# Kernel optimization log

Hardware: AMD Instinct MI355X
Metric: run time of the kernel (lower is better)

## Reference

```python
import jax, jax.numpy as jnp
import numpy as np

B, S, N, IN_DIM = 64, 12, 170, 1
E, L, C, H, OUT = 128, 4, 2, 8, 1
OFFSET, PAD = 0, 1          # seq_offset=0 -> Conv2d padding (0,1)
LOOKUP, MAXLEN = 0, 100
EPS = 1e-5


def _shift(x, s):
    """y[:, i] = x[:, i+s] along axis 1, zero padded."""
    if s == 0:
        return x
    z = jnp.zeros_like(x[:, :abs(s)])
    if s > 0:
        return jnp.concatenate([x[:, s:], z], axis=1)
    return jnp.concatenate([z, x[:, :s]], axis=1)


def _masked_conv_diag(x, w):
    """Diagonal of Conv2d(kernel=(1,3), pad=(0,PAD)) applied to the causally
    masked repeated tensor, computed directly without the O(B*S*S*E) blowup:
      out[b,i] = sum_k W[:,:,k] @ (mask(i, i+k-PAD) * x[b, i+k-PAD])
    where mask(i,j) = (j <= i) or (j < OFFSET)."""
    i = jnp.arange(x.shape[1])
    out = None
    for k in range(3):
        s = k - PAD
        term = jnp.einsum('bse,oe->bso', _shift(x, s), w[:, :, k])
        if s > 0:  # only future taps can be masked out
            term = term * (i + s < OFFSET).astype(x.dtype)[None, :, None]
        out = term if out is None else out + term
    return out


def _conv1d_k3(x, w, b):
    """Conv1d over the seq dim, kernel 3, padding 1, with bias. x:[b,s,e]."""
    out = b
    for k in range(3):
        out = out + jnp.einsum('bse,oe->bso', _shift(x, k - 1), w[:, :, k])
    return out


def _layer_norm(x, g, b):
    m = jnp.mean(x, -1, keepdims=True)
    v = jnp.mean((x - m) ** 2, -1, keepdims=True)
    return (x - m) * jax.lax.rsqrt(v + EPS) * g + b


def _mha(q_in, kv_in, w, b, mask=None):
    dh = E // H
    q = (q_in @ w[0] + b[0]).reshape(q_in.shape[0], q_in.shape[1], H, dh)
    k = (kv_in @ w[1] + b[1]).reshape(kv_in.shape[0], kv_in.shape[1], H, dh)
    v = (kv_in @ w[2] + b[2]).reshape(kv_in.shape[0], kv_in.shape[1], H, dh)
    s = jnp.einsum('bqhd,bkhd->bhqk', q, k) * np.float32(1.0 / np.sqrt(dh))
    if mask is not None:
        s = jnp.where(mask[None, None], s, jnp.float32(-1e9))
    a = jax.nn.softmax(s, axis=-1)
    o = jnp.einsum('bhqk,bkhd->bqhd', a, v).reshape(q_in.shape[0], q_in.shape[1], E)
    return o @ w[3] + b[3]


def setup_inputs() -> dict:
    key = jax.random.key(0)
    ks = jax.random.split(key, 16)

    def nrm(k, shape, scale=0.05):
        return scale * jax.random.normal(k, shape, dtype=jnp.float32)

    # sinusoidal positional table, length MAXLEN
    pos = np.arange(MAXLEN)[:, None].astype(np.float32)
    div = np.exp(-np.log(10000.0) * np.arange(0, E, 2) / E).astype(np.float32)
    pe = np.zeros((MAXLEN, E), np.float32)
    pe[:, 0::2] = np.sin(pos * div)
    pe[:, 1::2] = np.cos(pos * div)

    return {
        'x': jax.random.normal(ks[0], (B, S, N, IN_DIM), jnp.float32),
        'enc_x': jax.random.normal(ks[1], (C, B * N, S, E), jnp.float32),
        'tgt_mask': jnp.tril(jnp.ones((S, S), bool)),
        'emb_w': nrm(ks[2], (IN_DIM, E), 1.0),
        'emb_b': jnp.zeros((E,), jnp.float32),
        'pe': jnp.asarray(pe),
        'conv_q_w': nrm(ks[3], (L, E, E, 3)),
        'conv_k_w': nrm(ks[4], (L, C, E, E, 3)),
        'conv_k_b': jnp.zeros((L, C, E), jnp.float32),
        'sa_w': nrm(ks[5], (L, 4, E, E)),
        'sa_b': jnp.zeros((L, 4, E), jnp.float32),
        'ca_w': nrm(ks[6], (L, C, 4, E, E)),
        'ca_b': jnp.zeros((L, C, 4, E), jnp.float32),
        'ff_w1': nrm(ks[7], (L, E, 4 * E)),
        'ff_b1': jnp.zeros((L, 4 * E), jnp.float32),
        'ff_w2': nrm(ks[8], (L, 4 * E, E)),
        'ff_b2': jnp.zeros((L, E), jnp.float32),
        'ln_g': jnp.ones((L, 3, E), jnp.float32),
        'ln_b': jnp.zeros((L, 3, E), jnp.float32),
        'fc_w': nrm(ks[9], (E, OUT)),
        'fc_b': jnp.zeros((OUT,), jnp.float32),
    }


def reference(x, enc_x, tgt_mask, emb_w, emb_b, pe, conv_q_w, conv_k_w, conv_k_b,
              sa_w, sa_b, ca_w, ca_b, ff_w1, ff_b1, ff_w2, ff_b2, ln_g, ln_b,
              fc_w, fc_b):
    h = x @ emb_w + emb_b                                    # [B,S,N,E]
    h = jnp.transpose(h, (1, 0, 2, 3)).reshape(S, B * N, E)  # [S,B*N,E]
    h = jnp.transpose(h, (1, 0, 2))                          # [B*N,S,E]
    h = h + pe[LOOKUP:LOOKUP + S]
    for l in range(L):
        # local trends: causal masked-conv query (the fused diagonal)
        h = _masked_conv_diag(h, conv_q_w[l])
        enc_list = [_conv1d_k3(enc_x[i], conv_k_w[l, i], conv_k_b[l, i])
                    for i in range(C)]
        # decoder block: self-attn -> cross-attn (avg over features) -> FFN
        h = _layer_norm(h + _mha(h, h, sa_w[l], sa_b[l], tgt_mask),
                        ln_g[l, 0], ln_b[l, 0])
        cross = sum(_mha(h, enc_list[i], ca_w[l, i], ca_b[l, i])
                    for i in range(C)) / C
        h = _layer_norm(h + cross, ln_g[l, 1], ln_b[l, 1])
        f = jax.nn.relu(h @ ff_w1[l] + ff_b1[l]) @ ff_w2[l] + ff_b2[l]
        h = _layer_norm(h + f, ln_g[l, 2], ln_b[l, 2])
    out = h @ fc_w + fc_b                                    # [B*N,S,OUT]
    out = jnp.transpose(out, (1, 0, 2)).reshape(S, B, N, OUT)
    return jnp.transpose(out, (1, 0, 2, 3))                  # [B,S,N,OUT]
```

## Files before the change

### kernel.cpp

```cpp
#include <hip/hip_runtime.h>


#define B_   64
#define S_   12
#define N_   170
#define BN_  (B_*N_)
#define E_   128
#define L_   4
#define C_   2
#define H_   8
#define DH_  16
#define FF_  512
#define EPS_ 1e-5f
#define THREADS 256

typedef unsigned short u16;
typedef __attribute__((ext_vector_type(4))) float f32x4;
typedef __attribute__((ext_vector_type(8))) u16   us8;
typedef __attribute__((ext_vector_type(4))) u16   us4;
typedef __attribute__((ext_vector_type(8))) __bf16 bf16x8;
union FragU { us8 u; bf16x8 b; };

__device__ __forceinline__ u16 f2bf(float f) {
    __bf16 h = (__bf16)f;
    return __builtin_bit_cast(u16, h);
}
__device__ __forceinline__ float bf2f(u16 s) {
    return __builtin_bit_cast(float, (unsigned)s << 16);
}

__global__ void k_encbf(const float* __restrict__ src, u16* __restrict__ dst, int n8) {
    int i = blockIdx.x * 256 + threadIdx.x;
    if (i < n8) {
        const f32x4 v0 = ((const f32x4*)src)[i*2];
        const f32x4 v1 = ((const f32x4*)src)[i*2 + 1];
        us8 w;
        w[0]=f2bf(v0[0]); w[1]=f2bf(v0[1]); w[2]=f2bf(v0[2]); w[3]=f2bf(v0[3]);
        w[4]=f2bf(v1[0]); w[5]=f2bf(v1[1]); w[6]=f2bf(v1[2]); w[7]=f2bf(v1[3]);
        ((us8*)dst)[i] = w;
    }
}

__global__ void k_wpack(const float* __restrict__ cq, const float* __restrict__ sa,
                        const float* __restrict__ ck, const float* __restrict__ ca,
                        const float* __restrict__ f1, const float* __restrict__ f2,
                        u16* __restrict__ wp) {
    int f  = blockIdx.x * 256 + threadIdx.x;
    int l  = f / 57344, fl = f % 57344;
    const float* src; int sk, so, KS, q;
    if (fl < 4096)        { int tap = fl >> 11; q = fl & 2047; KS = 4;
                            src = cq + (size_t)l*49152 + tap;            sk = 3;   so = 384; }
    else if (fl < 12288)  { int j = (fl - 4096) >> 11; q = fl & 2047; KS = 4;
                            src = sa + (size_t)(l*4 + j)*16384;          sk = 128; so = 1;   }
    else if (fl < 24576)  { int ct = (fl - 12288) >> 11; q = fl & 2047; KS = 4;
                            int ci = ct / 3, tap = ct % 3;
                            src = ck + (size_t)(l*2 + ci)*49152 + tap;   sk = 3;   so = 384; }
    else if (fl < 40960)  { int cj = (fl - 24576) >> 11; q = fl & 2047; KS = 4;
                            src = ca + (size_t)(l*8 + cj)*16384;         sk = 128; so = 1;   }
    else if (fl < 49152)  { q = fl - 40960; KS = 4;
                            src = f1 + (size_t)l*65536;                  sk = 512; so = 1;   }
    else                  { q = fl - 49152; KS = 16;
                            src = f2 + (size_t)l*65536;                  sk = 128; so = 1;   }
    int lane = q & 63, tt = q >> 6;
    int ks = tt % KS, ntile = tt / KS;
    int k0 = ks*32 + ((lane >> 4) << 3);
    int o  = ntile*16 + (lane & 15);
    us8 w;
    #pragma unroll
    for (int i = 0; i < 8; i++) w[i] = f2bf(src[(size_t)(k0 + i)*sk + (size_t)o*so]);
    *(us8*)(wp + (size_t)f*8) = w;
}

__device__ __forceinline__ void zero_pad_rows(u16* dst, int t) {
    if (t < 128) {
        int chunk = t & 15, ridx = t >> 4;
        int row = 12 + (ridx & 3) + ((ridx >> 2) << 4);
        us8 z = {0,0,0,0,0,0,0,0};
        *(us8*)((char*)dst + (((row << 8) + (chunk << 4)) ^ ((row & 7) << 4))) = z;
    }
}

__device__ __forceinline__ void stage24_bf(const u16* __restrict__ src, u16* dst, int t) {
    for (int i = t; i < 384; i += THREADS) {
        us8 v = ((const us8*)src)[i];
        int row = i >> 4;
        int g = row / 12, s = row - g*12;
        int rowT = g*16 + s;
        int colb = (i & 15) << 4;
        *(us8*)((char*)dst + (((rowT << 8) + colb) ^ ((rowT & 7) << 4))) = v;
    }
    zero_pad_rows(dst, t);
}

__device__ __forceinline__ void stage24_embed(const float* __restrict__ x,
    const float* __restrict__ ew, const float* __restrict__ eb,
    const float* __restrict__ pe, int bn0, u16* dst, int t) {
    #pragma unroll
    for (int it = 0; it < 3; it++) {
        int i = t + it*THREADS;
        int elem = i << 2;
        int srow = elem >> 7;
        int g = srow / 12, s = srow - g*12;
        int row = g*16 + s;
        int col = elem & 127;
        int bn = bn0 + g, b = bn / N_, n = bn - b*N_;
        float xv = x[(b*S_ + s)*N_ + n];
        const f32x4 w  = *(const f32x4*)(ew + col);
        const f32x4 bb = *(const f32x4*)(eb + col);
        const f32x4 p  = *(const f32x4*)(pe + s*E_ + col);
        us4 o; o[0] = f2bf(xv*w[0] + bb[0] + p[0]); o[1] = f2bf(xv*w[1] + bb[1] + p[1]);
               o[2] = f2bf(xv*w[2] + bb[2] + p[2]); o[3] = f2bf(xv*w[3] + bb[3] + p[3]);
        *(us4*)((char*)dst + (((row << 8) + (col << 1)) ^ ((row & 7) << 4))) = o;
    }
    zero_pad_rows(dst, t);
}

__device__ __forceinline__ void acc_init(f32x4 (&acc)[2][2], const float* bias, int wave, int lane) {
    #pragma unroll
    for (int nt = 0; nt < 2; nt++) {
        float bv = bias ? bias[(wave*2 + nt)*16 + (lane & 15)] : 0.f;
        #pragma unroll
        for (int mt = 0; mt < 2; mt++) {
            acc[mt][nt][0] = bv; acc[mt][nt][1] = bv; acc[mt][nt][2] = bv; acc[mt][nt][3] = bv;
        }
    }
}

__device__ __forceinline__ bf16x8 ldA(const u16* A, int row, int colb) {
    FragU fu; fu.u = *(const us8*)((const char*)A + (((row << 8) + colb) ^ ((row & 7) << 4)));
    return fu.b;
}

template<int KSTOT>
__device__ __forceinline__ void gemm24(const u16* A, const us8* __restrict__ WP, int ksOff,
                                       f32x4 (&acc)[2][2], int wave, int lane) {
    #pragma unroll
    for (int ks = 0; ks < 4; ks++) {
        int colb = (ks*32 + ((lane >> 4) << 3)) << 1;
        bf16x8 a[2];
        #pragma unroll
        for (int mt = 0; mt < 2; mt++) a[mt] = ldA(A, mt*16 + (lane & 15), colb);
        #pragma unroll
        for (int nt = 0; nt < 2; nt++) {
            FragU fb; fb.u = WP[((wave*2 + nt)*KSTOT + ksOff + ks)*64 + lane];
            #pragma unroll
            for (int mt = 0; mt < 2; mt++)
                acc[mt][nt] = __builtin_amdgcn_mfma_f32_16x16x32_bf16(a[mt], fb.b, acc[mt][nt], 0, 0, 0);
        }
    }
}

__device__ __forceinline__ void gemm24_rows(const u16* A, const int (&sr)[2],
                                            const us8* __restrict__ WP,
                                            f32x4 (&acc)[2][2], int wave, int lane) {
    #pragma unroll
    for (int ks = 0; ks < 4; ks++) {
        int colb = (ks*32 + ((lane >> 4) << 3)) << 1;
        bf16x8 a[2];
        #pragma unroll
        for (int mt = 0; mt < 2; mt++) a[mt] = ldA(A, sr[mt], colb);
        #pragma unroll
        for (int nt = 0; nt < 2; nt++) {
            FragU fb; fb.u = WP[((wave*2 + nt)*4 + ks)*64 + lane];
            #pragma unroll
            for (int mt = 0; mt < 2; mt++)
                acc[mt][nt] = __builtin_amdgcn_mfma_f32_16x16x32_bf16(a[mt], fb.b, acc[mt][nt], 0, 0, 0);
        }
    }
}

__device__ __forceinline__ void gemm24_x3(const u16* A,
        const us8* __restrict__ B0, const us8* __restrict__ B1, const us8* __restrict__ B2,
        f32x4 (&c0)[2][2], f32x4 (&c1)[2][2], f32x4 (&c2)[2][2], int wave, int lane) {
    #pragma unroll
    for (int ks = 0; ks < 4; ks++) {
        int colb = (ks*32 + ((lane >> 4) << 3)) << 1;
        bf16x8 a[2];
        #pragma unroll
        for (int mt = 0; mt < 2; mt++) a[mt] = ldA(A, mt*16 + (lane & 15), colb);
        #pragma unroll
        for (int nt = 0; nt < 2; nt++) {
            int bi = ((wave*2 + nt)*4 + ks)*64 + lane;
            FragU f0, f1, f2; f0.u = B0[bi]; f1.u = B1[bi]; f2.u = B2[bi];
            #pragma unroll
            for (int mt = 0; mt < 2; mt++) {
                c0[mt][nt] = __builtin_amdgcn_mfma_f32_16x16x32_bf16(a[mt], f0.b, c0[mt][nt], 0, 0, 0);
                c1[mt][nt] = __builtin_amdgcn_mfma_f32_16x16x32_bf16(a[mt], f1.b, c1[mt][nt], 0, 0, 0);
                c2[mt][nt] = __builtin_amdgcn_mfma_f32_16x16x32_bf16(a[mt], f2.b, c2[mt][nt], 0, 0, 0);
            }
        }
    }
}

__device__ __forceinline__ void gemm24_x2(const u16* A,
        const us8* __restrict__ B0, const us8* __restrict__ B1,
        f32x4 (&c0)[2][2], f32x4 (&c1)[2][2], int wave, int lane) {
    #pragma unroll
    for (int ks = 0; ks < 4; ks++) {
        int colb = (ks*32 + ((lane >> 4) << 3)) << 1;
        bf16x8 a[2];
        #pragma unroll
        for (int mt = 0; mt < 2; mt++) a[mt] = ldA(A, mt*16 + (lane & 15), colb);
        #pragma unroll
        for (int nt = 0; nt < 2; nt++) {
            int bi = ((wave*2 + nt)*4 + ks)*64 + lane;
            FragU f0, f1; f0.u = B0[bi]; f1.u = B1[bi];
            #pragma unroll
            for (int mt = 0; mt < 2; mt++) {
                c0[mt][nt] = __builtin_amdgcn_mfma_f32_16x16x32_bf16(a[mt], f0.b, c0[mt][nt], 0, 0, 0);
                c1[mt][nt] = __builtin_amdgcn_mfma_f32_16x16x32_bf16(a[mt], f1.b, c1[mt][nt], 0, 0, 0);
            }
        }
    }
}

template<bool RELU>
__device__ __forceinline__ void acc_store_bf(const f32x4 (&acc)[2][2], u16* Bp, int wave, int lane) {
    #pragma unroll
    for (int mt = 0; mt < 2; mt++)
    #pragma unroll
    for (int nt = 0; nt < 2; nt++)
    #pragma unroll
    for (int r = 0; r < 4; r++) {
        int row = mt*16 + ((lane >> 4) << 2) + r;
        int col = (wave*2 + nt)*16 + (lane & 15);
        float v = acc[mt][nt][r];
        if (RELU) v = fmaxf(v, 0.f);
        *(u16*)((char*)Bp + (((row << 8) + (col << 1)) ^ ((row & 7) << 4))) = f2bf(v);
    }
}

__device__ __forceinline__ void ld16(const u16* Bf, int row, int colb, float* o16) {
    int x = (row & 7) << 4;
    int base = (row << 8) + colb;
    us8 u0 = *(const us8*)((const char*)Bf + (base ^ x));
    us8 u1 = *(const us8*)((const char*)Bf + ((base + 16) ^ x));
    #pragma unroll
    for (int d = 0; d < 8; d++) { o16[d] = bf2f(u0[d]); o16[8+d] = bf2f(u1[d]); }
}

template<bool MASK>
__device__ __forceinline__ void attn24(u16* QA, const u16* KB, const u16* VB, int t) {
    if (t < 192) {
        int g = t / 96, rem = t % 96;
        int hh = rem / 12, qi = rem % 12;
        int hb2 = hh << 5;
        int rq = g*16 + qi;
        float qv[16]; ld16(QA, rq, hb2, qv);
        float sc[12]; float mx = -1e30f;
        #pragma unroll
        for (int j = 0; j < 12; j++) {
            float kv[16]; ld16(KB, g*16 + j, hb2, kv);
            float s = 0.f;
            #pragma unroll
            for (int d = 0; d < 16; d++) s += qv[d]*kv[d];
            s *= 0.25f;
            if (MASK && j > qi) s = -1e30f;
            sc[j] = s; mx = fmaxf(mx, s);
        }
        float sum = 0.f;
        #pragma unroll
        for (int j = 0; j < 12; j++) { sc[j] = __expf(sc[j] - mx); sum += sc[j]; }
        float inv = 1.f/sum;
        float ov[16];
        #pragma unroll
        for (int d = 0; d < 16; d++) ov[d] = 0.f;
        #pragma unroll
        for (int j = 0; j < 12; j++) {
            float vv[16]; ld16(VB, g*16 + j, hb2, vv);
            #pragma unroll
            for (int d = 0; d < 16; d++) ov[d] += sc[j]*vv[d];
        }
        int x = (rq & 7) << 4;
        us8 w0, w1;
        #pragma unroll
        for (int d = 0; d < 8; d++) { w0[d] = f2bf(ov[d]*inv); w1[d] = f2bf(ov[8+d]*inv); }
        *(us8*)((char*)QA + (((rq << 8) + hb2) ^ x))      = w0;
        *(us8*)((char*)QA + (((rq << 8) + hb2 + 16) ^ x)) = w1;
    }
}

__device__ __forceinline__ void ln_inreg(f32x4 (&v)[2][2], float* lnbuf,
                                         const float* __restrict__ g, const float* __restrict__ bb,
                                         int wave, int lane) {
    float gc[2], bc[2];
    #pragma unroll
    for (int nt = 0; nt < 2; nt++) {
        int col = (wave*2 + nt)*16 + (lane & 15);
        gc[nt] = g[col]; bc[nt] = bb[col];
    }
    #pragma unroll
    for (int mt = 0; mt < 2; mt++)
    #pragma unroll
    for (int r = 0; r < 4; r++) {
        float a = v[mt][0][r], c = v[mt][1][r];
        float p = a + c, q = a*a + c*c;
        #pragma unroll
        for (int off = 1; off < 16; off <<= 1) { p += __shfl_xor(p, off); q += __shfl_xor(q, off); }
        if ((lane & 15) == 0) {
            int row = mt*16 + ((lane >> 4) << 2) + r;
            lnbuf[(row*4 + wave)*2]     = p;
            lnbuf[(row*4 + wave)*2 + 1] = q;
        }
    }
    __syncthreads();
    #pragma unroll
    for (int mt = 0; mt < 2; mt++)
    #pragma unroll
    for (int r = 0; r < 4; r++) {
        int row = mt*16 + ((lane >> 4) << 2) + r;
        float sum = 0.f, ss = 0.f;
        #pragma unroll
        for (int w2 = 0; w2 < 4; w2++) { sum += lnbuf[(row*4 + w2)*2]; ss += lnbuf[(row*4 + w2)*2 + 1]; }
        float m   = sum * (1.f/128.f);
        float var = ss * (1.f/128.f) - m*m;
        float inv = rsqrtf(var + EPS_);
        #pragma unroll
        for (int nt = 0; nt < 2; nt++)
            v[mt][nt][r] = (v[mt][nt][r] - m)*inv*gc[nt] + bc[nt];
    }
}

template<bool EMB, bool FIN>
__global__ void __launch_bounds__(THREADS, 2)
k_layer(u16* __restrict__ hb, const float* __restrict__ x,
        const float* __restrict__ ew, const float* __restrict__ ebp, const float* __restrict__ pe,
        const u16* __restrict__ encb, const u16* __restrict__ lw,
        const float* __restrict__ sab, const float* __restrict__ ckb, const float* __restrict__ cab,
        const float* __restrict__ fb1, const float* __restrict__ fb2,
        const float* __restrict__ lg, const float* __restrict__ lb,
        const float* __restrict__ fcw, const float* __restrict__ fcb,
        float* __restrict__ outp) {
    __shared__ __align__(16) u16 P0[4096], P1[4096], P2[4096], P3[4096], P4[4096];
    float* lnbuf = (float*)P2;

    int t = threadIdx.x, wave = t >> 6, lane = t & 63;
    int bid = blockIdx.x;
    u16* hp = hb + (size_t)(bid*2) * (S_*E_);

    if (EMB) stage24_embed(x, ew, ebp, pe, bid*2, P0, t);
    else     stage24_bf(hp, P0, t);
    stage24_bf(encb + (size_t)(bid*2) * (S_*E_), P4, t);
    __syncthreads();

    int rr = lane & 15;
    int srp[2], srf[2], srn[2];
    #pragma unroll
    for (int mt = 0; mt < 2; mt++) {
        srp[mt] = (rr >= 1)     ? mt*16 + rr - 1 : mt*16 + 12;
        srf[mt] = mt*16 + rr;
        srn[mt] = (rr + 1 < 12) ? mt*16 + rr + 1 : mt*16 + 12;
    }

    f32x4 cacc[2][2];
    acc_init(cacc, nullptr, wave, lane);
    gemm24_rows(P0, srp, (const us8*)lw,           cacc, wave, lane);
    gemm24_rows(P0, srf, (const us8*)(lw + 16384), cacc, wave, lane);
    acc_store_bf<false>(cacc, P1, wave, lane);
    __syncthreads();

    {
        const us8* sap = (const us8*)(lw + 32768);
        f32x4 aq[2][2], ak[2][2], av[2][2];
        acc_init(aq, sab,       wave, lane);
        acc_init(ak, sab + 128, wave, lane);
        acc_init(av, sab + 256, wave, lane);
        gemm24_x3(P1, sap, sap + 2048, sap + 4096, aq, ak, av, wave, lane);
        acc_store_bf<false>(aq, P0, wave, lane);
        acc_store_bf<false>(ak, P2, wave, lane);
        acc_store_bf<false>(av, P3, wave, lane);
    }
    __syncthreads();
    attn24<true>(P0, P2, P3, t);
    __syncthreads();

    f32x4 hres[2][2];
    {
        f32x4 a[2][2];
        acc_init(a, sab + 384, wave, lane);
        gemm24<4>(P0, (const us8*)(lw + 81920), 0, a, wave, lane);
        #pragma unroll
        for (int mt = 0; mt < 2; mt++)
        #pragma unroll
        for (int nt = 0; nt < 2; nt++) hres[mt][nt] = a[mt][nt] + cacc[mt][nt];
    }
    ln_inreg(hres, lnbuf, lg, lb, wave, lane);
    acc_store_bf<false>(hres, P1, wave, lane);
    {
        const us8* ckp = (const us8*)(lw + 98304);
        f32x4 a[2][2];
        acc_init(a, ckb, wave, lane);
        gemm24_rows(P4, srp, ckp,        a, wave, lane);
        gemm24_rows(P4, srf, ckp + 2048, a, wave, lane);
        gemm24_rows(P4, srn, ckp + 4096, a, wave, lane);
        acc_store_bf<false>(a, P3, wave, lane);
    }
    __syncthreads();

    f32x4 creg[2][2];
    #pragma unroll
    for (int nt = 0; nt < 2; nt++) {
        int col = (wave*2 + nt)*16 + (lane & 15);
        float bv = cab[3*128 + col] + cab[7*128 + col];
        #pragma unroll
        for (int mt = 0; mt < 2; mt++) { creg[mt][nt][0]=bv; creg[mt][nt][1]=bv; creg[mt][nt][2]=bv; creg[mt][nt][3]=bv; }
    }

    const us8* cap0 = (const us8*)(lw + 196608);
    {
        f32x4 aq[2][2], ak[2][2], av[2][2];
        acc_init(aq, cab, wave, lane);
        gemm24<4>(P1, cap0, 0, aq, wave, lane);
        acc_store_bf<false>(aq, P0, wave, lane);
        acc_init(ak, cab + 128, wave, lane);
        acc_init(av, cab + 256, wave, lane);
        gemm24_x2(P3, cap0 + 2048, cap0 + 4096, ak, av, wave, lane);
        acc_store_bf<false>(ak, P2, wave, lane);
        acc_store_bf<false>(av, P4, wave, lane);
    }
    __syncthreads();
    stage24_bf(encb + ((size_t)BN_ + bid*2) * (S_*E_), P3, t);
    attn24<false>(P0, P2, P4, t);
    __syncthreads();

    gemm24<4>(P0, cap0 + 6144, 0, creg, wave, lane);
    {
        const us8* ckp = (const us8*)(lw + 98304 + 3*16384);
        f32x4 a[2][2];
        acc_init(a, ckb + 128, wave, lane);
        gemm24_rows(P3, srp, ckp,        a, wave, lane);
        gemm24_rows(P3, srf, ckp + 2048, a, wave, lane);
        gemm24_rows(P3, srn, ckp + 4096, a, wave, lane);
        acc_store_bf<false>(a, P4, wave, lane);
    }
    __syncthreads();

    const us8* cap1 = (const us8*)(lw + 196608 + 4*16384);
    {
        f32x4 aq[2][2], ak[2][2], av[2][2];
        acc_init(aq, cab + 4*128, wave, lane);
        gemm24<4>(P1, cap1, 0, aq, wave, lane);
        acc_store_bf<false>(aq, P0, wave, lane);
        acc_init(ak, cab + 5*128, wave, lane);
        acc_init(av, cab + 6*128, wave, lane);
        gemm24_x2(P4, cap1 + 2048, cap1 + 4096, ak, av, wave, lane);
        acc_store_bf<false>(ak, P2, wave, lane);
        acc_store_bf<false>(av, P3, wave, lane);
    }
    __syncthreads();
    attn24<false>(P0, P2, P3, t);
    __syncthreads();

    gemm24<4>(P0, cap1 + 6144, 0, creg, wave, lane);
    #pragma unroll
    for (int mt = 0; mt < 2; mt++)
    #pragma unroll
    for (int nt = 0; nt < 2; nt++) hres[mt][nt] = hres[mt][nt] + 0.5f*creg[mt][nt];
    ln_inreg(hres, lnbuf, lg + 128, lb + 128, wave, lane);
    acc_store_bf<false>(hres, P1, wave, lane);
    __syncthreads();

    f32x4 ffacc[2][2];
    acc_init(ffacc, fb2, wave, lane);
    #pragma unroll
    for (int half = 0; half < 2; half++) {
        {
            f32x4 a[2][2];
            acc_init(a, fb1 + (half*2)*128, wave, lane);
            gemm24<4>(P1, (const us8*)(lw + 327680) + (half*2)*2048, 0, a, wave, lane);
            acc_store_bf<true>(a, P2, wave, lane);
        }
        {
            f32x4 a[2][2];
            acc_init(a, fb1 + (half*2 + 1)*128, wave, lane);
            gemm24<4>(P1, (const us8*)(lw + 327680) + (half*2 + 1)*2048, 0, a, wave, lane);
            acc_store_bf<true>(a, P3, wave, lane);
        }
        __syncthreads();
        gemm24<16>(P2, (const us8*)(lw + 393216), (half*2)*4,     ffacc, wave, lane);
        gemm24<16>(P3, (const us8*)(lw + 393216), (half*2 + 1)*4, ffacc, wave, lane);
        __syncthreads();
    }
    #pragma unroll
    for (int mt = 0; mt < 2; mt++)
    #pragma unroll
    for (int nt = 0; nt < 2; nt++) hres[mt][nt] = hres[mt][nt] + ffacc[mt][nt];
    ln_inreg(hres, lnbuf, lg + 256, lb + 256, wave, lane);

    if (FIN) {
        float fw[2];
        #pragma unroll
        for (int nt = 0; nt < 2; nt++) fw[nt] = fcw[(wave*2 + nt)*16 + (lane & 15)];
        float pr[2][4];
        #pragma unroll
        for (int mt = 0; mt < 2; mt++)
        #pragma unroll
        for (int r = 0; r < 4; r++) {
            float p = hres[mt][0][r]*fw[0] + hres[mt][1][r]*fw[1];
            #pragma unroll
            for (int off = 1; off < 16; off <<= 1) p += __shfl_xor(p, off);
            pr[mt][r] = p;
        }
        __syncthreads();
        if ((lane & 15) == 0) {
            #pragma unroll
            for (int mt = 0; mt < 2; mt++)
            #pragma unroll
            for (int r = 0; r < 4; r++) {
                int row = mt*16 + ((lane >> 4) << 2) + r;
                lnbuf[row*4 + wave] = pr[mt][r];
            }
        }
        __syncthreads();
        if (t < 24) {
            int g = t / 12, s = t % 12;
            int row = g*16 + s;
            float s4 = lnbuf[row*4] + lnbuf[row*4+1] + lnbuf[row*4+2] + lnbuf[row*4+3] + fcb[0];
            int bn = bid*2 + g;
            int b = bn / N_, n = bn - b*N_;
            outp[(b*S_ + s)*N_ + n] = s4;
        }
    } else {
        #pragma unroll
        for (int mt = 0; mt < 2; mt++)
        #pragma unroll
        for (int r = 0; r < 4; r++) {
            int row = ((lane >> 4) << 2) + r;
            if (row < 12) {
                #pragma unroll
                for (int nt = 0; nt < 2; nt++) {
                    int col = (wave*2 + nt)*16 + (lane & 15);
                    hp[(mt*S_ + row)*E_ + col] = f2bf(hres[mt][nt][r]);
                }
            }
        }
    }
}

extern "C" void kernel_launch(void* const* d_in, const int* in_sizes, int n_in,
                              void* d_out, int out_size, void* d_ws, size_t ws_size,
                              hipStream_t stream) {
    const float* x        = (const float*)d_in[0];
    const float* enc_x    = (const float*)d_in[1];
    const float* emb_w    = (const float*)d_in[3];
    const float* emb_b    = (const float*)d_in[4];
    const float* pe       = (const float*)d_in[5];
    const float* conv_q_w = (const float*)d_in[6];
    const float* conv_k_w = (const float*)d_in[7];
    const float* conv_k_b = (const float*)d_in[8];
    const float* sa_w     = (const float*)d_in[9];
    const float* sa_b     = (const float*)d_in[10];
    const float* ca_w     = (const float*)d_in[11];
    const float* ca_b     = (const float*)d_in[12];
    const float* ff_w1    = (const float*)d_in[13];
    const float* ff_b1    = (const float*)d_in[14];
    const float* ff_w2    = (const float*)d_in[15];
    const float* ff_b2    = (const float*)d_in[16];
    const float* ln_g     = (const float*)d_in[17];
    const float* ln_b     = (const float*)d_in[18];
    const float* fc_w     = (const float*)d_in[19];
    const float* fc_b     = (const float*)d_in[20];

    const size_t HN = (size_t)BN_ * S_ * E_;
    u16* hb   = (u16*)d_ws;
    u16* encb = hb + HN;
    u16* wpk  = encb + 2*HN;

    {
        int n8 = (int)(2*HN/8);
        k_encbf<<<(n8 + 255)/256, 256, 0, stream>>>(enc_x, encb, n8);
    }
    k_wpack<<<896, 256, 0, stream>>>(conv_q_w, sa_w, conv_k_w, ca_w, ff_w1, ff_w2, wpk);

    for (int l = 0; l < L_; l++) {
        const u16* lw = wpk + (size_t)l*458752;
        const float* sab = sa_b + l*512;
        const float* ckb = conv_k_b + l*256;
        const float* cab = ca_b + l*1024;
        const float* fb1 = ff_b1 + l*512;
        const float* fb2 = ff_b2 + l*128;
        const float* lg  = ln_g + l*384;
        const float* lb  = ln_b + l*384;
        if (l == 0)
            k_layer<true, false><<<BN_/2, THREADS, 0, stream>>>(hb, x, emb_w, emb_b, pe, encb, lw,
                sab, ckb, cab, fb1, fb2, lg, lb, fc_w, fc_b, (float*)d_out);
        else if (l == L_-1)
            k_layer<false, true><<<BN_/2, THREADS, 0, stream>>>(hb, x, emb_w, emb_b, pe, encb, lw,
                sab, ckb, cab, fb1, fb2, lg, lb, fc_w, fc_b, (float*)d_out);
        else
            k_layer<false, false><<<BN_/2, THREADS, 0, stream>>>(hb, x, emb_w, emb_b, pe, encb, lw,
                sab, ckb, cab, fb1, fb2, lg, lb, fc_w, fc_b, (float*)d_out);
    }
}
```

Before: 1.522 ms.

## Pack four sequences per block into 48 dense rows instead of two padded

Each block now handles four (b,n) sequences laid out as 48 contiguous rows (3 MFMA M-tiles) instead of two sequences padded to 32 rows. This removes the padding waste (24 useful of 32 rows becomes 48 of 48) and halves the grid, so each weight fragment loaded from global memory feeds more MFMAs. Conv shifts across sequence boundaries now read from a zero row buffer, and attention indexes rows by g*12. The cost is more accumulator registers and more LDS per block, which may reduce occupancy.

```diff
diff --git a/kernel.cpp b/kernel.cpp
--- a/kernel.cpp
+++ b/kernel.cpp
@@ -71,38 +71,27 @@
     *(us8*)(wp + (size_t)f*8) = w;
 }
 
-__device__ __forceinline__ void zero_pad_rows(u16* dst, int t) {
-    if (t < 128) {
-        int chunk = t & 15, ridx = t >> 4;
-        int row = 12 + (ridx & 3) + ((ridx >> 2) << 4);
-        us8 z = {0,0,0,0,0,0,0,0};
-        *(us8*)((char*)dst + (((row << 8) + (chunk << 4)) ^ ((row & 7) << 4))) = z;
-    }
-}
-
-__device__ __forceinline__ void stage24_bf(const u16* __restrict__ src, u16* dst, int t) {
-    for (int i = t; i < 384; i += THREADS) {
+__device__ __forceinline__ void stage48_bf(const u16* __restrict__ src, u16* dst, int t) {
+    #pragma unroll
+    for (int it = 0; it < 3; it++) {
+        int i = t + it*THREADS;
         us8 v = ((const us8*)src)[i];
         int row = i >> 4;
-        int g = row / 12, s = row - g*12;
-        int rowT = g*16 + s;
         int colb = (i & 15) << 4;
-        *(us8*)((char*)dst + (((rowT << 8) + colb) ^ ((rowT & 7) << 4))) = v;
-    }
-    zero_pad_rows(dst, t);
-}
-
-__device__ __forceinline__ void stage24_embed(const float* __restrict__ x,
+        *(us8*)((char*)dst + (((row << 8) + colb) ^ ((row & 7) << 4))) = v;
+    }
+}
+
+__device__ __forceinline__ void stage48_embed(const float* __restrict__ x,
     const float* __restrict__ ew, const float* __restrict__ eb,
     const float* __restrict__ pe, int bn0, u16* dst, int t) {
     #pragma unroll
-    for (int it = 0; it < 3; it++) {
+    for (int it = 0; it < 6; it++) {
         int i = t + it*THREADS;
         int elem = i << 2;
-        int srow = elem >> 7;
-        int g = srow / 12, s = srow - g*12;
-        int row = g*16 + s;
+        int row = elem >> 7;
         int col = elem & 127;
+        int g = row / 12, s = row - g*12;
         int bn = bn0 + g, b = bn / N_, n = bn - b*N_;
         float xv = x[(b*S_ + s)*N_ + n];
         const f32x4 w  = *(const f32x4*)(ew + col);
@@ -112,15 +101,14 @@
                o[2] = f2bf(xv*w[2] + bb[2] + p[2]); o[3] = f2bf(xv*w[3] + bb[3] + p[3]);
         *(us4*)((char*)dst + (((row << 8) + (col << 1)) ^ ((row & 7) << 4))) = o;
     }
-    zero_pad_rows(dst, t);
-}
-
-__device__ __forceinline__ void acc_init(f32x4 (&acc)[2][2], const float* bias, int wave, int lane) {
+}
+
+__device__ __forceinline__ void acc_init(f32x4 (&acc)[3][2], const float* bias, int wave, int lane) {
     #pragma unroll
     for (int nt = 0; nt < 2; nt++) {
         float bv = bias ? bias[(wave*2 + nt)*16 + (lane & 15)] : 0.f;
         #pragma unroll
-        for (int mt = 0; mt < 2; mt++) {
+        for (int mt = 0; mt < 3; mt++) {
             acc[mt][nt][0] = bv; acc[mt][nt][1] = bv; acc[mt][nt][2] = bv; acc[mt][nt][3] = bv;
         }
     }
@@ -132,58 +120,64 @@
 }
 
 template<int KSTOT>
-__device__ __forceinline__ void gemm24(const u16* A, const us8* __restrict__ WP, int ksOff,
-                                       f32x4 (&acc)[2][2], int wave, int lane) {
+__device__ __forceinline__ void gemm48(const u16* A, const us8* __restrict__ WP, int ksOff,
+                                       f32x4 (&acc)[3][2], int wave, int lane) {
     #pragma unroll
     for (int ks = 0; ks < 4; ks++) {
         int colb = (ks*32 + ((lane >> 4) << 3)) << 1;
-        bf16x8 a[2];
-        #pragma unroll
-        for (int mt = 0; mt < 2; mt++) a[mt] = ldA(A, mt*16 + (lane & 15), colb);
+        bf16x8 a[3];
+        #pragma unroll
+        for (int mt = 0; mt < 3; mt++) a[mt] = ldA(A, mt*16 + (lane & 15), colb);
         #pragma unroll
         for (int nt = 0; nt < 2; nt++) {
             FragU fb; fb.u = WP[((wave*2 + nt)*KSTOT + ksOff + ks)*64 + lane];
             #pragma unroll
-            for (int mt = 0; mt < 2; mt++)
+            for (int mt = 0; mt < 3; mt++)
                 acc[mt][nt] = __builtin_amdgcn_mfma_f32_16x16x32_bf16(a[mt], fb.b, acc[mt][nt], 0, 0, 0);
         }
     }
 }
 
-__device__ __forceinline__ void gemm24_rows(const u16* A, const int (&sr)[2],
+__device__ __forceinline__ void gemm48_rows(const u16* A, const u16* ZR, const int (&sr)[3],
                                             const us8* __restrict__ WP,
-                                            f32x4 (&acc)[2][2], int wave, int lane) {
+                                            f32x4 (&acc)[3][2], int wave, int lane) {
     #pragma unroll
     for (int ks = 0; ks < 4; ks++) {
         int colb = (ks*32 + ((lane >> 4) << 3)) << 1;
-        bf16x8 a[2];
-        #pragma unroll
-        for (int mt = 0; mt < 2; mt++) a[mt] = ldA(A, sr[mt], colb);
+        bf16x8 a[3];
+        #pragma unroll
+        for (int mt = 0; mt < 3; mt++) {
+            const char* p = (sr[mt] >= 0)
+                ? (const char*)A + (((sr[mt] << 8) + colb) ^ ((sr[mt] & 7) << 4))
+                : (const char*)ZR + colb;
+            FragU fu; fu.u = *(const us8*)p;
+            a[mt] = fu.b;
+        }
         #pragma unroll
         for (int nt = 0; nt < 2; nt++) {
             FragU fb; fb.u = WP[((wave*2 + nt)*4 + ks)*64 + lane];
             #pragma unroll
-            for (int mt = 0; mt < 2; mt++)
+            for (int mt = 0; mt < 3; mt++)
                 acc[mt][nt] = __builtin_amdgcn_mfma_f32_16x16x32_bf16(a[mt], fb.b, acc[mt][nt], 0, 0, 0);
         }
     }
 }
 
-__device__ __forceinline__ void gemm24_x3(const u16* A,
+__device__ __forceinline__ void gemm48_x3(const u16* A,
         const us8* __restrict__ B0, const us8* __restrict__ B1, const us8* __restrict__ B2,
-        f32x4 (&c0)[2][2], f32x4 (&c1)[2][2], f32x4 (&c2)[2][2], int wave, int lane) {
+        f32x4 (&c0)[3][2], f32x4 (&c1)[3][2], f32x4 (&c2)[3][2], int wave, int lane) {
     #pragma unroll
     for (int ks = 0; ks < 4; ks++) {
         int colb = (ks*32 + ((lane >> 4) << 3)) << 1;
-        bf16x8 a[2];
-        #pragma unroll
-        for (int mt = 0; mt < 2; mt++) a[mt] = ldA(A, mt*16 + (lane & 15), colb);
+        bf16x8 a[3];
+        #pragma unroll
+        for (int mt = 0; mt < 3; mt++) a[mt] = ldA(A, mt*16 + (lane & 15), colb);
         #pragma unroll
         for (int nt = 0; nt < 2; nt++) {
             int bi = ((wave*2 + nt)*4 + ks)*64 + lane;
             FragU f0, f1, f2; f0.u = B0[bi]; f1.u = B1[bi]; f2.u = B2[bi];
             #pragma unroll
-            for (int mt = 0; mt < 2; mt++) {
+            for (int mt = 0; mt < 3; mt++) {
                 c0[mt][nt] = __builtin_amdgcn_mfma_f32_16x16x32_bf16(a[mt], f0.b, c0[mt][nt], 0, 0, 0);
                 c1[mt][nt] = __builtin_amdgcn_mfma_f32_16x16x32_bf16(a[mt], f1.b, c1[mt][nt], 0, 0, 0);
                 c2[mt][nt] = __builtin_amdgcn_mfma_f32_16x16x32_bf16(a[mt], f2.b, c2[mt][nt], 0, 0, 0);
@@ -192,21 +186,21 @@
     }
 }
 
-__device__ __forceinline__ void gemm24_x2(const u16* A,
+__device__ __forceinline__ void gemm48_x2(const u16* A,
         const us8* __restrict__ B0, const us8* __restrict__ B1,
-        f32x4 (&c0)[2][2], f32x4 (&c1)[2][2], int wave, int lane) {
+        f32x4 (&c0)[3][2], f32x4 (&c1)[3][2], int wave, int lane) {
     #pragma unroll
     for (int ks = 0; ks < 4; ks++) {
         int colb = (ks*32 + ((lane >> 4) << 3)) << 1;
-        bf16x8 a[2];
-        #pragma unroll
-        for (int mt = 0; mt < 2; mt++) a[mt] = ldA(A, mt*16 + (lane & 15), colb);
+        bf16x8 a[3];
+        #pragma unroll
+        for (int mt = 0; mt < 3; mt++) a[mt] = ldA(A, mt*16 + (lane & 15), colb);
         #pragma unroll
         for (int nt = 0; nt < 2; nt++) {
             int bi = ((wave*2 + nt)*4 + ks)*64 + lane;
             FragU f0, f1; f0.u = B0[bi]; f1.u = B1[bi];
             #pragma unroll
-            for (int mt = 0; mt < 2; mt++) {
+            for (int mt = 0; mt < 3; mt++) {
                 c0[mt][nt] = __builtin_amdgcn_mfma_f32_16x16x32_bf16(a[mt], f0.b, c0[mt][nt], 0, 0, 0);
                 c1[mt][nt] = __builtin_amdgcn_mfma_f32_16x16x32_bf16(a[mt], f1.b, c1[mt][nt], 0, 0, 0);
             }
@@ -215,9 +209,9 @@
 }
 
 template<bool RELU>
-__device__ __forceinline__ void acc_store_bf(const f32x4 (&acc)[2][2], u16* Bp, int wave, int lane) {
-    #pragma unroll
-    for (int mt = 0; mt < 2; mt++)
+__device__ __forceinline__ void acc_store_bf(const f32x4 (&acc)[3][2], u16* Bp, int wave, int lane) {
+    #pragma unroll
+    for (int mt = 0; mt < 3; mt++)
     #pragma unroll
     for (int nt = 0; nt < 2; nt++)
     #pragma unroll
@@ -240,47 +234,51 @@
 }
 
 template<bool MASK>
-__device__ __forceinline__ void attn24(u16* QA, const u16* KB, const u16* VB, int t) {
-    if (t < 192) {
-        int g = t / 96, rem = t % 96;
-        int hh = rem / 12, qi = rem % 12;
-        int hb2 = hh << 5;
-        int rq = g*16 + qi;
-        float qv[16]; ld16(QA, rq, hb2, qv);
-        float sc[12]; float mx = -1e30f;
-        #pragma unroll
-        for (int j = 0; j < 12; j++) {
-            float kv[16]; ld16(KB, g*16 + j, hb2, kv);
-            float s = 0.f;
-            #pragma unroll
-            for (int d = 0; d < 16; d++) s += qv[d]*kv[d];
-            s *= 0.25f;
-            if (MASK && j > qi) s = -1e30f;
-            sc[j] = s; mx = fmaxf(mx, s);
-        }
-        float sum = 0.f;
-        #pragma unroll
-        for (int j = 0; j < 12; j++) { sc[j] = __expf(sc[j] - mx); sum += sc[j]; }
-        float inv = 1.f/sum;
-        float ov[16];
-        #pragma unroll
-        for (int d = 0; d < 16; d++) ov[d] = 0.f;
-        #pragma unroll
-        for (int j = 0; j < 12; j++) {
-            float vv[16]; ld16(VB, g*16 + j, hb2, vv);
-            #pragma unroll
-            for (int d = 0; d < 16; d++) ov[d] += sc[j]*vv[d];
-        }
-        int x = (rq & 7) << 4;
-        us8 w0, w1;
-        #pragma unroll
-        for (int d = 0; d < 8; d++) { w0[d] = f2bf(ov[d]*inv); w1[d] = f2bf(ov[8+d]*inv); }
-        *(us8*)((char*)QA + (((rq << 8) + hb2) ^ x))      = w0;
-        *(us8*)((char*)QA + (((rq << 8) + hb2 + 16) ^ x)) = w1;
-    }
-}
-
-__device__ __forceinline__ void ln_inreg(f32x4 (&v)[2][2], float* lnbuf,
+__device__ __forceinline__ void attn48(u16* QA, const u16* KB, const u16* VB, int t) {
+    #pragma unroll
+    for (int it = 0; it < 2; it++) {
+        int task = t + it*THREADS;
+        if (task < 384) {
+            int g = task / 96, rem = task % 96;
+            int hh = rem / 12, qi = rem % 12;
+            int hb2 = hh << 5;
+            int rq = g*12 + qi;
+            float qv[16]; ld16(QA, rq, hb2, qv);
+            float sc[12]; float mx = -1e30f;
+            #pragma unroll
+            for (int j = 0; j < 12; j++) {
+                float kv[16]; ld16(KB, g*12 + j, hb2, kv);
+                float s = 0.f;
+                #pragma unroll
+                for (int d = 0; d < 16; d++) s += qv[d]*kv[d];
+                s *= 0.25f;
+                if (MASK && j > qi) s = -1e30f;
+                sc[j] = s; mx = fmaxf(mx, s);
+            }
+            float sum = 0.f;
+            #pragma unroll
+            for (int j = 0; j < 12; j++) { sc[j] = __expf(sc[j] - mx); sum += sc[j]; }
+            float inv = 1.f/sum;
+            float ov[16];
+            #pragma unroll
+            for (int d = 0; d < 16; d++) ov[d] = 0.f;
+            #pragma unroll
+            for (int j = 0; j < 12; j++) {
+                float vv[16]; ld16(VB, g*12 + j, hb2, vv);
+                #pragma unroll
+                for (int d = 0; d < 16; d++) ov[d] += sc[j]*vv[d];
+            }
+            int x = (rq & 7) << 4;
+            us8 w0, w1;
+            #pragma unroll
+            for (int d = 0; d < 8; d++) { w0[d] = f2bf(ov[d]*inv); w1[d] = f2bf(ov[8+d]*inv); }
+            *(us8*)((char*)QA + (((rq << 8) + hb2) ^ x))      = w0;
+            *(us8*)((char*)QA + (((rq << 8) + hb2 + 16) ^ x)) = w1;
+        }
+    }
+}
+
+__device__ __forceinline__ void ln_inreg(f32x4 (&v)[3][2], float* lnbuf,
                                          const float* __restrict__ g, const float* __restrict__ bb,
                                          int wave, int lane) {
     float gc[2], bc[2];
@@ -290,7 +288,7 @@
         gc[nt] = g[col]; bc[nt] = bb[col];
     }
     #pragma unroll
-    for (int mt = 0; mt < 2; mt++)
+    for (int mt = 0; mt < 3; mt++)
     #pragma unroll
     for (int r = 0; r < 4; r++) {
         float a = v[mt][0][r], c = v[mt][1][r];
@@ -305,7 +303,7 @@
     }
     __syncthreads();
     #pragma unroll
-    for (int mt = 0; mt < 2; mt++)
+    for (int mt = 0; mt < 3; mt++)
     #pragma unroll
     for (int r = 0; r < 4; r++) {
         int row = mt*16 + ((lane >> 4) << 2) + r;
@@ -331,56 +329,59 @@
         const float* __restrict__ lg, const float* __restrict__ lb,
         const float* __restrict__ fcw, const float* __restrict__ fcb,
         float* __restrict__ outp) {
-    __shared__ __align__(16) u16 P0[4096], P1[4096], P2[4096], P3[4096], P4[4096];
+    __shared__ __align__(16) u16 P0[6144], P1[6144], P2[6144], P3[6144], P4[6144], ZR[128];
     float* lnbuf = (float*)P2;
 
     int t = threadIdx.x, wave = t >> 6, lane = t & 63;
     int bid = blockIdx.x;
-    u16* hp = hb + (size_t)(bid*2) * (S_*E_);
-
-    if (EMB) stage24_embed(x, ew, ebp, pe, bid*2, P0, t);
-    else     stage24_bf(hp, P0, t);
-    stage24_bf(encb + (size_t)(bid*2) * (S_*E_), P4, t);
-    __syncthreads();
-
-    int rr = lane & 15;
-    int srp[2], srf[2], srn[2];
-    #pragma unroll
-    for (int mt = 0; mt < 2; mt++) {
-        srp[mt] = (rr >= 1)     ? mt*16 + rr - 1 : mt*16 + 12;
-        srf[mt] = mt*16 + rr;
-        srn[mt] = (rr + 1 < 12) ? mt*16 + rr + 1 : mt*16 + 12;
-    }
-
-    f32x4 cacc[2][2];
+    u16* hp = hb + (size_t)(bid*4) * (S_*E_);
+
+    if (t < 64) ((unsigned*)ZR)[t] = 0;
+    if (EMB) stage48_embed(x, ew, ebp, pe, bid*4, P0, t);
+    else     stage48_bf(hp, P0, t);
+    stage48_bf(encb + (size_t)(bid*4) * (S_*E_), P4, t);
+    __syncthreads();
+
+    int gg[3], rr[3];
+    #pragma unroll
+    for (int mt = 0; mt < 3; mt++) { int m = mt*16 + (lane & 15); gg[mt] = m/12; rr[mt] = m - gg[mt]*12; }
+    int srp[3], srf[3], srn[3];
+    #pragma unroll
+    for (int mt = 0; mt < 3; mt++) {
+        srp[mt] = (rr[mt] >= 1)     ? gg[mt]*12 + rr[mt] - 1 : -1;
+        srf[mt] = gg[mt]*12 + rr[mt];
+        srn[mt] = (rr[mt] + 1 < 12) ? gg[mt]*12 + rr[mt] + 1 : -1;
+    }
+
+    f32x4 cacc[3][2];
     acc_init(cacc, nullptr, wave, lane);
-    gemm24_rows(P0, srp, (const us8*)lw,           cacc, wave, lane);
-    gemm24_rows(P0, srf, (const us8*)(lw + 16384), cacc, wave, lane);
+    gemm48_rows(P0, ZR, srp, (const us8*)lw,           cacc, wave, lane);
+    gemm48_rows(P0, ZR, srf, (const us8*)(lw + 16384), cacc, wave, lane);
     acc_store_bf<false>(cacc, P1, wave, lane);
     __syncthreads();
 
     {
         const us8* sap = (const us8*)(lw + 32768);
-        f32x4 aq[2][2], ak[2][2], av[2][2];
+        f32x4 aq[3][2], ak[3][2], av[3][2];
         acc_init(aq, sab,       wave, lane);
         acc_init(ak, sab + 128, wave, lane);
         acc_init(av, sab + 256, wave, lane);
-        gemm24_x3(P1, sap, sap + 2048, sap + 4096, aq, ak, av, wave, lane);
+        gemm48_x3(P1, sap, sap + 2048, sap + 4096, aq, ak, av, wave, lane);
         acc_store_bf<false>(aq, P0, wave, lane);
         acc_store_bf<false>(ak, P2, wave, lane);
         acc_store_bf<false>(av, P3, wave, lane);
     }
     __syncthreads();
-    attn24<true>(P0, P2, P3, t);
-    __syncthreads();
-
-    f32x4 hres[2][2];
-    {
-        f32x4 a[2][2];
+    attn48<true>(P0, P2, P3, t);
+    __syncthreads();
+
+    f32x4 hres[3][2];
+    {
+        f32x4 a[3][2];
         acc_init(a, sab + 384, wave, lane);
-        gemm24<4>(P0, (const us8*)(lw + 81920), 0, a, wave, lane);
-        #pragma unroll
-        for (int mt = 0; mt < 2; mt++)
+        gemm48<4>(P0, (const us8*)(lw + 81920), 0, a, wave, lane);
+        #pragma unroll
+        for (int mt = 0; mt < 3; mt++)
         #pragma unroll
         for (int nt = 0; nt < 2; nt++) hres[mt][nt] = a[mt][nt] + cacc[mt][nt];
     }
@@ -388,101 +389,101 @@
     acc_store_bf<false>(hres, P1, wave, lane);
     {
         const us8* ckp = (const us8*)(lw + 98304);
-        f32x4 a[2][2];
+        f32x4 a[3][2];
         acc_init(a, ckb, wave, lane);
-        gemm24_rows(P4, srp, ckp,        a, wave, lane);
-        gemm24_rows(P4, srf, ckp + 2048, a, wave, lane);
-        gemm24_rows(P4, srn, ckp + 4096, a, wave, lane);
+        gemm48_rows(P4, ZR, srp, ckp,        a, wave, lane);
+        gemm48_rows(P4, ZR, srf, ckp + 2048, a, wave, lane);
+        gemm48_rows(P4, ZR, srn, ckp + 4096, a, wave, lane);
         acc_store_bf<false>(a, P3, wave, lane);
     }
     __syncthreads();
 
-    f32x4 creg[2][2];
+    f32x4 creg[3][2];
     #pragma unroll
     for (int nt = 0; nt < 2; nt++) {
         int col = (wave*2 + nt)*16 + (lane & 15);
         float bv = cab[3*128 + col] + cab[7*128 + col];
         #pragma unroll
-        for (int mt = 0; mt < 2; mt++) { creg[mt][nt][0]=bv; creg[mt][nt][1]=bv; creg[mt][nt][2]=bv; creg[mt][nt][3]=bv; }
+        for (int mt = 0; mt < 3; mt++) { creg[mt][nt][0]=bv; creg[mt][nt][1]=bv; creg[mt][nt][2]=bv; creg[mt][nt][3]=bv; }
     }
 
     const us8* cap0 = (const us8*)(lw + 196608);
     {
-        f32x4 aq[2][2], ak[2][2], av[2][2];
+        f32x4 aq[3][2], ak[3][2], av[3][2];
         acc_init(aq, cab, wave, lane);
-        gemm24<4>(P1, cap0, 0, aq, wave, lane);
+        gemm48<4>(P1, cap0, 0, aq, wave, lane);
         acc_store_bf<false>(aq, P0, wave, lane);
         acc_init(ak, cab + 128, wave, lane);
         acc_init(av, cab + 256, wave, lane);
-        gemm24_x2(P3, cap0 + 2048, cap0 + 4096, ak, av, wave, lane);
+        gemm48_x2(P3, cap0 + 2048, cap0 + 4096, ak, av, wave, lane);
         acc_store_bf<false>(ak, P2, wave, lane);
         acc_store_bf<false>(av, P4, wave, lane);
     }
     __syncthreads();
-    stage24_bf(encb + ((size_t)BN_ + bid*2) * (S_*E_), P3, t);
-    attn24<false>(P0, P2, P4, t);
-    __syncthreads();
-
-    gemm24<4>(P0, cap0 + 6144, 0, creg, wave, lane);
+    stage48_bf(encb + ((size_t)BN_ + bid*4) * (S_*E_), P3, t);
+    attn48<false>(P0, P2, P4, t);
+    __syncthreads();
+
+    gemm48<4>(P0, cap0 + 6144, 0, creg, wave, lane);
     {
         const us8* ckp = (const us8*)(lw + 98304 + 3*16384);
-        f32x4 a[2][2];
+        f32x4 a[3][2];
         acc_init(a, ckb + 128, wave, lane);
-        gemm24_rows(P3, srp, ckp,        a, wave, lane);
-        gemm24_rows(P3, srf, ckp + 2048, a, wave, lane);
-        gemm24_rows(P3, srn, ckp + 4096, a, wave, lane);
+        gemm48_rows(P3, ZR, srp, ckp,        a, wave, lane);
+        gemm48_rows(P3, ZR, srf, ckp + 2048, a, wave, lane);
+        gemm48_rows(P3, ZR, srn, ckp + 4096, a, wave, lane);
         acc_store_bf<false>(a, P4, wave, lane);
     }
     __syncthreads();
 
     const us8* cap1 = (const us8*)(lw + 196608 + 4*16384);
     {
-        f32x4 aq[2][2], ak[2][2], av[2][2];
+        f32x4 aq[3][2], ak[3][2], av[3][2];
         acc_init(aq, cab + 4*128, wave, lane);
-        gemm24<4>(P1, cap1, 0, aq, wave, lane);
+        gemm48<4>(P1, cap1, 0, aq, wave, lane);
         acc_store_bf<false>(aq, P0, wave, lane);
         acc_init(ak, cab + 5*128, wave, lane);
         acc_init(av, cab + 6*128, wave, lane);
-        gemm24_x2(P4, cap1 + 2048, cap1 + 4096, ak, av, wave, lane);
+        gemm48_x2(P4, cap1 + 2048, cap1 + 4096, ak, av, wave, lane);
         acc_store_bf<false>(ak, P2, wave, lane);
         acc_store_bf<false>(av, P3, wave, lane);
     }
     __syncthreads();
-    attn24<false>(P0, P2, P3, t);
-    __syncthreads();
-
-    gemm24<4>(P0, cap1 + 6144, 0, creg, wave, lane);
-    #pragma unroll
-    for (int mt = 0; mt < 2; mt++)
+    attn48<false>(P0, P2, P3, t);
+    __syncthreads();
+
+    gemm48<4>(P0, cap1 + 6144, 0, creg, wave, lane);
+    #pragma unroll
+    for (int mt = 0; mt < 3; mt++)
     #pragma unroll
     for (int nt = 0; nt < 2; nt++) hres[mt][nt] = hres[mt][nt] + 0.5f*creg[mt][nt];
     ln_inreg(hres, lnbuf, lg + 128, lb + 128, wave, lane);
     acc_store_bf<false>(hres, P1, wave, lane);
     __syncthreads();
 
-    f32x4 ffacc[2][2];
+    f32x4 ffacc[3][2];
     acc_init(ffacc, fb2, wave, lane);
     #pragma unroll
     for (int half = 0; half < 2; half++) {
         {
-            f32x4 a[2][2];
+            f32x4 a[3][2];
             acc_init(a, fb1 + (half*2)*128, wave, lane);
-            gemm24<4>(P1, (const us8*)(lw + 327680) + (half*2)*2048, 0, a, wave, lane);
+            gemm48<4>(P1, (const us8*)(lw + 327680) + (half*2)*2048, 0, a, wave, lane);
             acc_store_bf<true>(a, P2, wave, lane);
         }
         {
-            f32x4 a[2][2];
+            f32x4 a[3][2];
             acc_init(a, fb1 + (half*2 + 1)*128, wave, lane);
-            gemm24<4>(P1, (const us8*)(lw + 327680) + (half*2 + 1)*2048, 0, a, wave, lane);
+            gemm48<4>(P1, (const us8*)(lw + 327680) + (half*2 + 1)*2048, 0, a, wave, lane);
             acc_store_bf<true>(a, P3, wave, lane);
         }
         __syncthreads();
-        gemm24<16>(P2, (const us8*)(lw + 393216), (half*2)*4,     ffacc, wave, lane);
-        gemm24<16>(P3, (const us8*)(lw + 393216), (half*2 + 1)*4, ffacc, wave, lane);
+        gemm48<16>(P2, (const us8*)(lw + 393216), (half*2)*4,     ffacc, wave, lane);
+        gemm48<16>(P3, (const us8*)(lw + 393216), (half*2 + 1)*4, ffacc, wave, lane);
         __syncthreads();
     }
     #pragma unroll
-    for (int mt = 0; mt < 2; mt++)
+    for (int mt = 0; mt < 3; mt++)
     #pragma unroll
     for (int nt = 0; nt < 2; nt++) hres[mt][nt] = hres[mt][nt] + ffacc[mt][nt];
     ln_inreg(hres, lnbuf, lg + 256, lb + 256, wave, lane);
@@ -491,9 +492,9 @@
         float fw[2];
         #pragma unroll
         for (int nt = 0; nt < 2; nt++) fw[nt] = fcw[(wave*2 + nt)*16 + (lane & 15)];
-        float pr[2][4];
-        #pragma unroll
-        for (int mt = 0; mt < 2; mt++)
+        float pr[3][4];
+        #pragma unroll
+        for (int mt = 0; mt < 3; mt++)
         #pragma unroll
         for (int r = 0; r < 4; r++) {
             float p = hres[mt][0][r]*fw[0] + hres[mt][1][r]*fw[1];
@@ -504,7 +505,7 @@
         __syncthreads();
         if ((lane & 15) == 0) {
             #pragma unroll
-            for (int mt = 0; mt < 2; mt++)
+            for (int mt = 0; mt < 3; mt++)
             #pragma unroll
             for (int r = 0; r < 4; r++) {
                 int row = mt*16 + ((lane >> 4) << 2) + r;
@@ -512,27 +513,22 @@
             }
         }
         __syncthreads();
-        if (t < 24) {
-            int g = t / 12, s = t % 12;
-            int row = g*16 + s;
-            float s4 = lnbuf[row*4] + lnbuf[row*4+1] + lnbuf[row*4+2] + lnbuf[row*4+3] + fcb[0];
-            int bn = bid*2 + g;
+        if (t < 48) {
+            float s4 = lnbuf[t*4] + lnbuf[t*4+1] + lnbuf[t*4+2] + lnbuf[t*4+3] + fcb[0];
+            int bn = bid*4 + t/12, s = t % 12;
             int b = bn / N_, n = bn - b*N_;
             outp[(b*S_ + s)*N_ + n] = s4;
         }
     } else {
         #pragma unroll
-        for (int mt = 0; mt < 2; mt++)
+        for (int mt = 0; mt < 3; mt++)
+        #pragma unroll
+        for (int nt = 0; nt < 2; nt++)
         #pragma unroll
         for (int r = 0; r < 4; r++) {
-            int row = ((lane >> 4) << 2) + r;
-            if (row < 12) {
-                #pragma unroll
-                for (int nt = 0; nt < 2; nt++) {
-                    int col = (wave*2 + nt)*16 + (lane & 15);
-                    hp[(mt*S_ + row)*E_ + col] = f2bf(hres[mt][nt][r]);
-                }
-            }
+            int row = mt*16 + ((lane >> 4) << 2) + r;
+            int col = (wave*2 + nt)*16 + (lane & 15);
+            hp[row*E_ + col] = f2bf(hres[mt][nt][r]);
         }
     }
 }
@@ -582,13 +578,13 @@
         const float* lg  = ln_g + l*384;
         const float* lb  = ln_b + l*384;
         if (l == 0)
-            k_layer<true, false><<<BN_/2, THREADS, 0, stream>>>(hb, x, emb_w, emb_b, pe, encb, lw,
+            k_layer<true, false><<<BN_/4, THREADS, 0, stream>>>(hb, x, emb_w, emb_b, pe, encb, lw,
                 sab, ckb, cab, fb1, fb2, lg, lb, fc_w, fc_b, (float*)d_out);
         else if (l == L_-1)
-            k_layer<false, true><<<BN_/2, THREADS, 0, stream>>>(hb, x, emb_w, emb_b, pe, encb, lw,
+            k_layer<false, true><<<BN_/4, THREADS, 0, stream>>>(hb, x, emb_w, emb_b, pe, encb, lw,
                 sab, ckb, cab, fb1, fb2, lg, lb, fc_w, fc_b, (float*)d_out);
         else
-            k_layer<false, false><<<BN_/2, THREADS, 0, stream>>>(hb, x, emb_w, emb_b, pe, encb, lw,
+            k_layer<false, false><<<BN_/4, THREADS, 0, stream>>>(hb, x, emb_w, emb_b, pe, encb, lw,
                 sab, ckb, cab, fb1, fb2, lg, lb, fc_w, fc_b, (float*)d_out);
     }
 }
```

Measured after the change: 1.606 ms. 5.6% more time.
